# Performance work log

Hardware: AMD Instinct MI355X
Metric: run time of the kernel (lower is better)

The kernel has to match this reference:

```python
import jax, jax.numpy as jnp
import numpy as np

B, S, D = 4, 2048, 2048
H = 16
Q_LORA = 1536
KV_LORA = 512
D_NOPE = 128
D_ROPE = 64
D_V = 128
MLP = 8192
EPS = 1e-6
THETA = 10000.0


def rmsnorm(x, scale, eps=EPS):
    var = jnp.mean(jnp.square(x.astype(jnp.float32)), axis=-1, keepdims=True)
    return (x * jax.lax.rsqrt(var + eps)).astype(x.dtype) * scale


def rope(x, positions):
    # x: [B, S, H, d], positions: [B, S]
    d = x.shape[-1]
    inv_freq = 1.0 / (THETA ** (jnp.arange(0, d, 2, dtype=jnp.float32) / d))
    ang = positions.astype(jnp.float32)[..., None] * inv_freq  # [B,S,d/2]
    cos = jnp.cos(ang)[:, :, None, :]
    sin = jnp.sin(ang)[:, :, None, :]
    x1, x2 = jnp.split(x, 2, axis=-1)
    return jnp.concatenate([x1 * cos - x2 * sin, x2 * cos + x1 * sin], axis=-1)


def setup_inputs() -> dict:
    key = jax.random.key(0)
    ks = jax.random.split(key, 16)
    sd = lambda fan: 1.0 / np.sqrt(fan)
    inp = {
        'inputs': jax.random.normal(ks[0], (B, S, D), jnp.float32),
        'decoder_segment_ids': jnp.ones((B, S), jnp.int32),
        'decoder_positions': jnp.broadcast_to(jnp.arange(S, dtype=jnp.int32), (B, S)),
        'pre_ln_scale': jnp.ones((D,), jnp.float32),
        'post_ln_scale': jnp.ones((D,), jnp.float32),
        'q_ln_scale': jnp.ones((Q_LORA,), jnp.float32),
        'kv_ln_scale': jnp.ones((KV_LORA,), jnp.float32),
        'wq_a': jax.random.normal(ks[1], (D, Q_LORA), jnp.float32) * sd(D),
        'wq_b': jax.random.normal(ks[2], (Q_LORA, H, D_NOPE + D_ROPE), jnp.float32) * sd(Q_LORA),
        'wkv_a': jax.random.normal(ks[3], (D, KV_LORA + D_ROPE), jnp.float32) * sd(D),
        'wkv_b': jax.random.normal(ks[4], (KV_LORA, H, D_NOPE + D_V), jnp.float32) * sd(KV_LORA),
        'wo_attn': jax.random.normal(ks[5], (H, D_V, D), jnp.float32) * sd(H * D_V),
        'wi_0': jax.random.normal(ks[6], (D, MLP), jnp.float32) * sd(D),
        'wi_1': jax.random.normal(ks[7], (D, MLP), jnp.float32) * sd(D),
        'wo_mlp': jax.random.normal(ks[8], (MLP, D), jnp.float32) * sd(MLP),
    }
    return inp


def reference(inputs, decoder_segment_ids, decoder_positions, pre_ln_scale, post_ln_scale,
              q_ln_scale, kv_ln_scale, wq_a, wq_b, wkv_a, wkv_b, wo_attn, wi_0, wi_1, wo_mlp):
    # ---- pre-norm ----
    lnx = rmsnorm(inputs, pre_ln_scale)

    # ---- MLA attention ----
    # low-rank query: down-proj, norm, up-proj
    q_c = rmsnorm(lnx @ wq_a, q_ln_scale)                       # [B,S,Q_LORA]
    q = jnp.einsum('bsr,rhd->bshd', q_c, wq_b)                  # [B,S,H,nope+rope]
    q_nope, q_rope = q[..., :D_NOPE], q[..., D_NOPE:]

    # compressed kv + decoupled rope key
    kv = lnx @ wkv_a                                            # [B,S,KV_LORA+rope]
    c_kv = rmsnorm(kv[..., :KV_LORA], kv_ln_scale)
    k_rope = kv[..., KV_LORA:][:, :, None, :]                   # [B,S,1,rope]
    kvu = jnp.einsum('bsr,rhd->bshd', c_kv, wkv_b)              # [B,S,H,nope+v]
    k_nope, v = kvu[..., :D_NOPE], kvu[..., D_NOPE:]

    q_rope = rope(q_rope, decoder_positions)
    k_rope = rope(k_rope, decoder_positions)
    k_rope = jnp.broadcast_to(k_rope, (B, S, H, D_ROPE))

    qf = jnp.concatenate([q_nope, q_rope], axis=-1)             # [B,S,H,192]
    kf = jnp.concatenate([k_nope, k_rope], axis=-1)

    scale = 1.0 / np.sqrt(D_NOPE + D_ROPE)
    scores = jnp.einsum('bqhd,bkhd->bhqk', qf, kf) * scale      # [B,H,S,S]

    pos = decoder_positions
    seg = decoder_segment_ids
    mask = (pos[:, :, None] >= pos[:, None, :]) & (seg[:, :, None] == seg[:, None, :])
    scores = jnp.where(mask[:, None, :, :], scores, -1e9)
    probs = jax.nn.softmax(scores, axis=-1)

    attn = jnp.einsum('bhqk,bkhd->bqhd', probs, v)              # [B,S,H,D_V]
    attn_out = jnp.einsum('bqhd,hdm->bqm', attn, wo_attn)       # [B,S,D]

    # ---- residual + post-norm ----
    intermediate = inputs + attn_out
    hidden = rmsnorm(intermediate, post_ln_scale)

    # ---- gated MLP (silu * linear) ----
    mlp = (jax.nn.silu(hidden @ wi_0) * (hidden @ wi_1)) @ wo_mlp

    return mlp + intermediate
```

## Files before the change

kernel.cpp:

```cpp
#include <hip/hip_runtime.h>
#include <stdint.h>

typedef unsigned short u16;
typedef __bf16 bf16x8 __attribute__((ext_vector_type(8)));
typedef float f32x4 __attribute__((ext_vector_type(4)));

#define B_ 4
#define S_ 2048
#define H_ 16
#define TOK (B_*S_)
#define MFMA_B16 __builtin_amdgcn_mfma_f32_16x16x32_bf16

__device__ __forceinline__ u16 f32_bf16(float f) {
    union { float f; unsigned int u; } x; x.f = f;
    return (u16)((x.u + 0x7fffu + ((x.u >> 16) & 1u)) >> 16);
}
__device__ __forceinline__ float bf2f(u16 v) {
    union { unsigned int u; float f; } x; x.u = ((unsigned int)v) << 16; return x.f;
}
__device__ __forceinline__ void gld_lds16(const u16* g, u16* lds) {
    __builtin_amdgcn_global_load_lds(
        (const __attribute__((address_space(1))) unsigned int*)g,
        (__attribute__((address_space(3))) unsigned int*)lds, 16, 0, 0);
}

__global__ void fill_sentinel(float* o, int n) {
    int i = blockIdx.x * 256 + threadIdx.x;
    if (i < n) o[i] = 12345.0f;
}

__global__ __launch_bounds__(256) void transpose_f32_bf16(const float* __restrict__ in, u16* __restrict__ out,
                                                          int K, int N, int Npad) {
    __shared__ float t[32][33];
    int nb = blockIdx.x * 32, kb = blockIdx.y * 32;
    int c = threadIdx.x & 31, r = threadIdx.x >> 5;
#pragma unroll
    for (int i = 0; i < 4; ++i) {
        int kk = kb + r + i * 8, nn = nb + c;
        t[r + i * 8][c] = (kk < K && nn < N) ? in[(size_t)kk * N + nn] : 0.f;
    }
    __syncthreads();
#pragma unroll
    for (int i = 0; i < 4; ++i) {
        int no = nb + r + i * 8, ko = kb + c;
        if (no < Npad && ko < K) out[(size_t)no * K + ko] = f32_bf16(t[c][r + i * 8]);
    }
}

__global__ __launch_bounds__(256) void rmsnorm_f32(const float* __restrict__ in, const float* __restrict__ sc,
                                                   u16* __restrict__ out, int N) {
    int row = blockIdx.x;
    const float* x = in + (size_t)row * N;
    float ss = 0.f;
    for (int c = threadIdx.x * 4; c < N; c += 1024) {
        float4 v = *(const float4*)(x + c);
        ss += v.x * v.x + v.y * v.y + v.z * v.z + v.w * v.w;
    }
#pragma unroll
    for (int off = 32; off; off >>= 1) ss += __shfl_down(ss, off);
    __shared__ float red[4];
    if ((threadIdx.x & 63) == 0) red[threadIdx.x >> 6] = ss;
    __syncthreads();
    float rs = rsqrtf((red[0] + red[1] + red[2] + red[3]) / (float)N + 1e-6f);
    for (int c = threadIdx.x * 4; c < N; c += 1024) {
        float4 v = *(const float4*)(x + c);
        float4 s4 = *(const float4*)(sc + c);
        ushort4 ov;
        ov.x = f32_bf16(v.x * rs * s4.x);
        ov.y = f32_bf16(v.y * rs * s4.y);
        ov.z = f32_bf16(v.z * rs * s4.z);
        ov.w = f32_bf16(v.w * rs * s4.w);
        *(ushort4*)&out[(size_t)row * N + c] = ov;
    }
}

__global__ __launch_bounds__(256) void rmsnorm_bf16(const u16* __restrict__ in, const float* __restrict__ sc,
                                                    u16* __restrict__ out, int N) {
    int row = blockIdx.x;
    const u16* x = in + (size_t)row * N;
    float ss = 0.f;
    for (int c = threadIdx.x * 8; c < N; c += 2048) {
        ushort4 v0 = *(const ushort4*)(x + c);
        ushort4 v1 = *(const ushort4*)(x + c + 4);
        float f0 = bf2f(v0.x), f1 = bf2f(v0.y), f2 = bf2f(v0.z), f3 = bf2f(v0.w);
        float f4 = bf2f(v1.x), f5 = bf2f(v1.y), f6 = bf2f(v1.z), f7 = bf2f(v1.w);
        ss += f0*f0 + f1*f1 + f2*f2 + f3*f3 + f4*f4 + f5*f5 + f6*f6 + f7*f7;
    }
#pragma unroll
    for (int off = 32; off; off >>= 1) ss += __shfl_down(ss, off);
    __shared__ float red[4];
    if ((threadIdx.x & 63) == 0) red[threadIdx.x >> 6] = ss;
    __syncthreads();
    float rs = rsqrtf((red[0] + red[1] + red[2] + red[3]) / (float)N + 1e-6f);
    for (int c = threadIdx.x * 8; c < N; c += 2048) {
        ushort4 v0 = *(const ushort4*)(x + c);
        ushort4 v1 = *(const ushort4*)(x + c + 4);
        ushort4 o0, o1;
        o0.x = f32_bf16(bf2f(v0.x) * rs * sc[c + 0]);
        o0.y = f32_bf16(bf2f(v0.y) * rs * sc[c + 1]);
        o0.z = f32_bf16(bf2f(v0.z) * rs * sc[c + 2]);
        o0.w = f32_bf16(bf2f(v0.w) * rs * sc[c + 3]);
        o1.x = f32_bf16(bf2f(v1.x) * rs * sc[c + 4]);
        o1.y = f32_bf16(bf2f(v1.y) * rs * sc[c + 5]);
        o1.z = f32_bf16(bf2f(v1.z) * rs * sc[c + 6]);
        o1.w = f32_bf16(bf2f(v1.w) * rs * sc[c + 7]);
        *(ushort4*)&out[(size_t)row * N + c] = o0;
        *(ushort4*)&out[(size_t)row * N + c + 4] = o1;
    }
}

__global__ __launch_bounds__(128) void kv_post(const u16* __restrict__ kv, const float* __restrict__ scale,
                                               const int* __restrict__ pos, u16* __restrict__ ckv,
                                               u16* __restrict__ kr) {
    int row = blockIdx.x;
    const u16* x = kv + (size_t)row * 640;
    int c = threadIdx.x * 4;
    ushort4 v = *(const ushort4*)(x + c);
    float f0 = bf2f(v.x), f1 = bf2f(v.y), f2 = bf2f(v.z), f3 = bf2f(v.w);
    float ss = f0*f0 + f1*f1 + f2*f2 + f3*f3;
#pragma unroll
    for (int off = 32; off; off >>= 1) ss += __shfl_down(ss, off);
    __shared__ float red[2];
    if ((threadIdx.x & 63) == 0) red[threadIdx.x >> 6] = ss;
    __syncthreads();
    float rs = rsqrtf((red[0] + red[1]) * (1.f / 512.f) + 1e-6f);
    float4 s4 = *(const float4*)(scale + c);
    ushort4 ov;
    ov.x = f32_bf16(f0 * rs * s4.x);
    ov.y = f32_bf16(f1 * rs * s4.y);
    ov.z = f32_bf16(f2 * rs * s4.z);
    ov.w = f32_bf16(f3 * rs * s4.w);
    *(ushort4*)&ckv[(size_t)row * 512 + c] = ov;
    if (threadIdx.x < 32) {
        int i = threadIdx.x;
        float x1 = bf2f(x[512 + i]), x2 = bf2f(x[544 + i]);
        float inv = expf(-(float)(2 * i) * (1.f / 64.f) * 9.2103403719761836f);
        float ang = (float)pos[row] * inv;
        float sn, cs; sincosf(ang, &sn, &cs);
        kr[(size_t)row * 64 + i]      = f32_bf16(x1 * cs - x2 * sn);
        kr[(size_t)row * 64 + 32 + i] = f32_bf16(x2 * cs + x1 * sn);
    }
}

__global__ __launch_bounds__(64) void q_rope_inplace(u16* __restrict__ q, const int* __restrict__ pos) {
    int token = blockIdx.x, h = blockIdx.y;
    u16* p = q + ((size_t)token * 16 + h) * 192;
    int t = threadIdx.x, i = t & 31;
    float x1 = bf2f(p[128 + i]), x2 = bf2f(p[160 + i]);
    float inv = expf(-(float)(2 * i) * (1.f / 64.f) * 9.2103403719761836f);
    float ang = (float)pos[token] * inv;
    float sn, cs; sincosf(ang, &sn, &cs);
    float val = (t < 32) ? (x1 * cs - x2 * sn) : (x2 * cs + x1 * sn);
    p[128 + t] = f32_bf16(val);
}

__global__ __launch_bounds__(320) void kv_build(const u16* __restrict__ kvu, const u16* __restrict__ kr,
                                                u16* __restrict__ kf, u16* __restrict__ vf, int tok0) {
    int local = blockIdx.x, h = blockIdx.y;
    int token = tok0 + local;
    int b = token >> 11, s = token & 2047;
    int bh = b * 16 + h;
    int tile = s >> 6, ki = s & 63;
    const u16* u = kvu + ((size_t)local * 16 + h) * 256;
    int t = threadIdx.x;
    if (t < 192) {
        u16 val = (t < 128) ? u[t] : kr[(size_t)token * 64 + (t - 128)];
        int byte = (ki * 384 + t * 2) ^ ((ki & 7) << 4);
        kf[(size_t)bh * (S_ * 192) + (size_t)tile * 12288 + (byte >> 1)] = val;
    } else {
        int dv = t - 192;
        u16 val = u[128 + dv];
        int byte = (dv * 128 + ki * 2) ^ ((dv & 7) << 4);
        vf[(size_t)bh * (S_ * 128) + (size_t)tile * 8192 + (byte >> 1)] = val;
    }
}

__global__ __launch_bounds__(256) void gemm128(const u16* __restrict__ A, const u16* __restrict__ Bt,
                                               u16* __restrict__ C, int M, int N, int K) {
    __shared__ u16 As[128 * 32];
    __shared__ u16 Bs[128 * 32];
    const int l = threadIdx.x & 63, w = threadIdx.x >> 6;
    const int wr = w >> 1, wc = w & 1;
    const int m0 = blockIdx.y * 128, n0 = blockIdx.x * 128;
    const int lm = l & 15, lg = l >> 4;
    const int srow = l >> 2, sk = (l & 3) * 8;
    f32x4 acc[4][4] = {};
    for (int k0 = 0; k0 < K; k0 += 32) {
#pragma unroll
        for (int i = 0; i < 2; ++i) {
            int c = w * 2 + i;
            gld_lds16(A  + (size_t)(m0 + c * 16 + srow) * K + k0 + sk, &As[c * 512]);
            gld_lds16(Bt + (size_t)(n0 + c * 16 + srow) * K + k0 + sk, &Bs[c * 512]);
        }
        __syncthreads();
        bf16x8 a[4], b[4];
#pragma unroll
        for (int m = 0; m < 4; ++m) a[m] = *(const bf16x8*)&As[(wr * 64 + m * 16 + lm) * 32 + lg * 8];
#pragma unroll
        for (int n = 0; n < 4; ++n) b[n] = *(const bf16x8*)&Bs[(wc * 64 + n * 16 + lm) * 32 + lg * 8];
#pragma unroll
        for (int m = 0; m < 4; ++m)
#pragma unroll
            for (int n = 0; n < 4; ++n)
                acc[m][n] = MFMA_B16(a[m], b[n], acc[m][n], 0, 0, 0);
        __syncthreads();
    }
#pragma unroll
    for (int m = 0; m < 4; ++m)
#pragma unroll
        for (int j = 0; j < 4; ++j) {
            int row = m0 + wr * 64 + m * 16 + lg * 4 + j;
            size_t base = (size_t)row * N + n0 + wc * 64;
#pragma unroll
            for (int n = 0; n < 4; ++n)
                C[base + n * 16 + lm] = f32_bf16(acc[m][n][j]);
        }
}

template<int EPI>
__global__ __launch_bounds__(512, 2) void gemm256(const u16* __restrict__ A, const u16* __restrict__ Bt,
                                                  void* __restrict__ Cv, const void* __restrict__ Rv,
                                                  int M, int N, int K) {
    __shared__ u16 lds[65536];
    char* ldsb = (char*)lds;
    const int tid = threadIdx.x;
    const int l = tid & 63, w = tid >> 6;
    const int wr = w >> 2, wcn = w & 3;
    const int lm = l & 15, lg = l >> 4;
    const int m0 = blockIdx.y * 256, n0 = blockIdx.x * 256;

    int gm[2], gk[2];
#pragma unroll
    for (int ld = 0; ld < 2; ++ld) {
        int P = tid * 16 + ld * 8192;
        int row = P >> 7;
        int un = (P & 127) ^ ((row & 7) << 4);
        gm[ld] = row * 2 + (un >> 6);
        gk[ld] = (un & 63) >> 1;
    }
    const u16* Ab = A + (size_t)m0 * K;
    const u16* Bb = Bt + (size_t)n0 * K;

    f32x4 acc[8][4] = {};

    auto stageA = [&](int t) {
#pragma unroll
        for (int ld = 0; ld < 2; ++ld)
            gld_lds16(Ab + (size_t)gm[ld] * K + t * 32 + gk[ld],
                      (u16*)(ldsb + (t & 3) * 32768 + tid * 16 + ld * 8192));
    };
    auto stageB = [&](int t) {
#pragma unroll
        for (int ld = 0; ld < 2; ++ld)
            gld_lds16(Bb + (size_t)gm[ld] * K + t * 32 + gk[ld],
                      (u16*)(ldsb + (t & 3) * 32768 + 16384 + tid * 16 + ld * 8192));
    };
    auto readA = [&](int buf, int fm) -> bf16x8 {
        int m = wr * 128 + fm * 16 + lm;
        int off = ((m & 1) * 64 + lg * 16) ^ (((m >> 1) & 7) << 4);
        return *(const bf16x8*)(ldsb + buf * 32768 + (m >> 1) * 128 + off);
    };
    auto readB = [&](int buf, int fn) -> bf16x8 {
        int n = wcn * 64 + fn * 16 + lm;
        int off = ((n & 1) * 64 + lg * 16) ^ (((n >> 1) & 7) << 4);
        return *(const bf16x8*)(ldsb + buf * 32768 + 16384 + (n >> 1) * 128 + off);
    };

    const int ntile = K >> 5;
    stageA(0); stageB(0);
    stageA(1); stageB(1);
    stageA(2); stageB(2);
    asm volatile("s_waitcnt vmcnt(8)" ::: "memory");
    __builtin_amdgcn_s_barrier();

#pragma unroll 1
    for (int t = 0; t < ntile; ++t) {
        const int buf = t & 3;
        bf16x8 b0 = readB(buf, 0), b1 = readB(buf, 1), b2 = readB(buf, 2), b3 = readB(buf, 3);
        bf16x8 a0 = readA(buf, 0), a1 = readA(buf, 1), a2 = readA(buf, 2), a3 = readA(buf, 3);
        if (t + 3 < ntile) stageA(t + 3);
        asm volatile("s_waitcnt lgkmcnt(0)" ::: "memory");
        __builtin_amdgcn_s_barrier();
        __builtin_amdgcn_sched_barrier(0);
        __builtin_amdgcn_s_setprio(1);
        acc[0][0] = MFMA_B16(a0, b0, acc[0][0], 0, 0, 0);
        acc[0][1] = MFMA_B16(a0, b1, acc[0][1], 0, 0, 0);
        acc[0][2] = MFMA_B16(a0, b2, acc[0][2], 0, 0, 0);
        acc[0][3] = MFMA_B16(a0, b3, acc[0][3], 0, 0, 0);
        acc[1][0] = MFMA_B16(a1, b0, acc[1][0], 0, 0, 0);
        acc[1][1] = MFMA_B16(a1, b1, acc[1][1], 0, 0, 0);
        acc[1][2] = MFMA_B16(a1, b2, acc[1][2], 0, 0, 0);
        acc[1][3] = MFMA_B16(a1, b3, acc[1][3], 0, 0, 0);
        acc[2][0] = MFMA_B16(a2, b0, acc[2][0], 0, 0, 0);
        acc[2][1] = MFMA_B16(a2, b1, acc[2][1], 0, 0, 0);
        acc[2][2] = MFMA_B16(a2, b2, acc[2][2], 0, 0, 0);
        acc[2][3] = MFMA_B16(a2, b3, acc[2][3], 0, 0, 0);
        acc[3][0] = MFMA_B16(a3, b0, acc[3][0], 0, 0, 0);
        acc[3][1] = MFMA_B16(a3, b1, acc[3][1], 0, 0, 0);
        acc[3][2] = MFMA_B16(a3, b2, acc[3][2], 0, 0, 0);
        acc[3][3] = MFMA_B16(a3, b3, acc[3][3], 0, 0, 0);
        __builtin_amdgcn_s_setprio(0);
        __builtin_amdgcn_s_barrier();
        a0 = readA(buf, 4); a1 = readA(buf, 5); a2 = readA(buf, 6); a3 = readA(buf, 7);
        if (t + 3 < ntile) stageB(t + 3);
        asm volatile("s_waitcnt lgkmcnt(0)" ::: "memory");
        if (t < ntile - 3)       { asm volatile("s_waitcnt vmcnt(8)" ::: "memory"); }
        else if (t == ntile - 3) { asm volatile("s_waitcnt vmcnt(4)" ::: "memory"); }
        else if (t == ntile - 2) { asm volatile("s_waitcnt vmcnt(0)" ::: "memory"); }
        __builtin_amdgcn_s_barrier();
        __builtin_amdgcn_sched_barrier(0);
        __builtin_amdgcn_s_setprio(1);
        acc[4][0] = MFMA_B16(a0, b0, acc[4][0], 0, 0, 0);
        acc[4][1] = MFMA_B16(a0, b1, acc[4][1], 0, 0, 0);
        acc[4][2] = MFMA_B16(a0, b2, acc[4][2], 0, 0, 0);
        acc[4][3] = MFMA_B16(a0, b3, acc[4][3], 0, 0, 0);
        acc[5][0] = MFMA_B16(a1, b0, acc[5][0], 0, 0, 0);
        acc[5][1] = MFMA_B16(a1, b1, acc[5][1], 0, 0, 0);
        acc[5][2] = MFMA_B16(a1, b2, acc[5][2], 0, 0, 0);
        acc[5][3] = MFMA_B16(a1, b3, acc[5][3], 0, 0, 0);
        acc[6][0] = MFMA_B16(a2, b0, acc[6][0], 0, 0, 0);
        acc[6][1] = MFMA_B16(a2, b1, acc[6][1], 0, 0, 0);
        acc[6][2] = MFMA_B16(a2, b2, acc[6][2], 0, 0, 0);
        acc[6][3] = MFMA_B16(a2, b3, acc[6][3], 0, 0, 0);
        acc[7][0] = MFMA_B16(a3, b0, acc[7][0], 0, 0, 0);
        acc[7][1] = MFMA_B16(a3, b1, acc[7][1], 0, 0, 0);
        acc[7][2] = MFMA_B16(a3, b2, acc[7][2], 0, 0, 0);
        acc[7][3] = MFMA_B16(a3, b3, acc[7][3], 0, 0, 0);
        __builtin_amdgcn_s_setprio(0);
        __builtin_amdgcn_s_barrier();
    }
#pragma unroll
    for (int fm = 0; fm < 8; ++fm)
#pragma unroll
        for (int j = 0; j < 4; ++j) {
            int row = m0 + wr * 128 + fm * 16 + lg * 4 + j;
            size_t base = (size_t)row * N + n0 + wcn * 64;
#pragma unroll
            for (int fn = 0; fn < 4; ++fn) {
                size_t idx = base + fn * 16 + lm;
                float v = acc[fm][fn][j];
                if (EPI == 0) {
                    ((u16*)Cv)[idx] = f32_bf16(v);
                } else if (EPI == 1) {
                    ((float*)Cv)[idx] = v + ((const float*)Rv)[idx];
                } else {
                    float x0 = bf2f(((const u16*)Rv)[idx]);
                    float sl = x0 / (1.f + expf(-x0));
                    ((u16*)Cv)[idx] = f32_bf16(sl * v);
                }
            }
        }
}

__global__ __launch_bounds__(256) void attn_fwd(const u16* __restrict__ qf, const u16* __restrict__ kfs,
                                                const u16* __restrict__ vfs, u16* __restrict__ attn) {
    __shared__ u16 Ks[64 * 192];
    __shared__ u16 Vs[128 * 64];
    __shared__ u16 Ps[4][1024];
    const int px = blockIdx.x;
    const int bh = blockIdx.y;
    const int b = bh >> 4, h = bh & 15;
    const int l = threadIdx.x & 63, w = threadIdx.x >> 6;
    const int lm = l & 15, g = l >> 4;
    const u16* kb0 = kfs + (size_t)bh * (S_ * 192);
    const u16* vb0 = vfs + (size_t)bh * (S_ * 128);
    const float scale = 0.07216878364870322f;

    for (int pass = 0; pass < 2; ++pass) {
        const int qb = pass ? (31 - px) : px;
        const int qrow = qb * 64 + w * 16 + lm;
        const u16* qp = qf + (((size_t)(b * S_ + qrow)) * 16 + h) * 192 + g * 8;
        bf16x8 qr[6];
#pragma unroll
        for (int c = 0; c < 6; ++c) qr[c] = *(const bf16x8*)(qp + c * 32);
        f32x4 o[8] = {};
        float mrow[4] = {-1e30f, -1e30f, -1e30f, -1e30f};
        float lrow[4] = {0.f, 0.f, 0.f, 0.f};
        for (int kt = 0; kt <= qb; ++kt) {
            const u16* kc = kb0 + (size_t)kt * 12288;
            const u16* vc = vb0 + (size_t)kt * 8192;
#pragma unroll
            for (int i = 0; i < 6; ++i) {
                int c = w + i * 4;
                gld_lds16(kc + c * 512 + l * 8, &Ks[c * 512]);
            }
#pragma unroll
            for (int i = 0; i < 4; ++i) {
                int c = w + i * 4;
                gld_lds16(vc + c * 512 + l * 8, &Vs[c * 512]);
            }
            __syncthreads();
            f32x4 sc[4] = {};
#pragma unroll
            for (int nf = 0; nf < 4; ++nf) {
                int key = nf * 16 + lm;
                int kswz = (key & 7) << 4;
#pragma unroll
                for (int c = 0; c < 6; ++c) {
                    int byte = (key * 384 + (c * 32 + g * 8) * 2) ^ kswz;
                    bf16x8 kv = *(const bf16x8*)((const char*)Ks + byte);
                    sc[nf] = MFMA_B16(qr[c], kv, sc[nf], 0, 0, 0);
                }
            }
#pragma unroll
            for (int j = 0; j < 4; ++j) {
                const int q_g = qb * 64 + w * 16 + g * 4 + j;
                float mx = -1e30f;
#pragma unroll
                for (int nf = 0; nf < 4; ++nf) {
                    int key_g = kt * 64 + nf * 16 + lm;
                    float v = sc[nf][j] * scale;
                    v = (key_g > q_g) ? -1e30f : v;
                    sc[nf][j] = v;
                    mx = fmaxf(mx, v);
                }
                mx = fmaxf(mx, __shfl_xor(mx, 1));
                mx = fmaxf(mx, __shfl_xor(mx, 2));
                mx = fmaxf(mx, __shfl_xor(mx, 4));
                mx = fmaxf(mx, __shfl_xor(mx, 8));
                float newm = fmaxf(mrow[j], mx);
                float fac = __expf(mrow[j] - newm);
                mrow[j] = newm;
                float rs = 0.f;
                u16 pb[4];
#pragma unroll
                for (int nf = 0; nf < 4; ++nf) {
                    float pv = __expf(sc[nf][j] - newm);
                    rs += pv;
                    pb[nf] = f32_bf16(pv);
                }
                rs += __shfl_xor(rs, 1);
                rs += __shfl_xor(rs, 2);
                rs += __shfl_xor(rs, 4);
                rs += __shfl_xor(rs, 8);
                lrow[j] = lrow[j] * fac + rs;
#pragma unroll
                for (int n = 0; n < 8; ++n) o[n][j] *= fac;
                int row = g * 4 + j;
                int rswz = (row & 7) << 4;
#pragma unroll
                for (int nf = 0; nf < 4; ++nf) {
                    int byte = (row * 128 + (nf * 16 + lm) * 2) ^ rswz;
                    *(u16*)((char*)&Ps[w][0] + byte) = pb[nf];
                }
            }
#pragma unroll
            for (int kc2 = 0; kc2 < 2; ++kc2) {
                int pbyte = (lm * 128 + (kc2 * 32 + g * 8) * 2) ^ ((lm & 7) << 4);
                bf16x8 pa = *(const bf16x8*)((const char*)&Ps[w][0] + pbyte);
#pragma unroll
                for (int n = 0; n < 8; ++n) {
                    int dv = n * 16 + lm;
                    int vbyte = (dv * 128 + (kc2 * 32 + g * 8) * 2) ^ ((dv & 7) << 4);
                    bf16x8 vv = *(const bf16x8*)((const char*)Vs + vbyte);
                    o[n] = MFMA_B16(pa, vv, o[n], 0, 0, 0);
                }
            }
            __syncthreads();
        }
#pragma unroll
        for (int j = 0; j < 4; ++j) {
            float inv = 1.f / lrow[j];
            int s = qb * 64 + w * 16 + g * 4 + j;
            size_t base = ((size_t)(b * S_ + s)) * (H_ * 128) + h * 128;
#pragma unroll
            for (int n = 0; n < 8; ++n)
                attn[base + n * 16 + lm] = f32_bf16(o[n][j] * inv);
        }
    }
}

extern "C" void kernel_launch(void* const* d_in, const int* in_sizes, int n_in,
                              void* d_out, int out_size, void* d_ws, size_t ws_size,
                              hipStream_t stream) {
    (void)in_sizes; (void)n_in;
    const float* inputs = (const float*)d_in[0];
    const int*   pos    = (const int*)d_in[2];
    const float* pre_s  = (const float*)d_in[3];
    const float* post_s = (const float*)d_in[4];
    const float* q_s    = (const float*)d_in[5];
    const float* kv_s   = (const float*)d_in[6];
    const float* wq_a   = (const float*)d_in[7];
    const float* wq_b   = (const float*)d_in[8];
    const float* wkv_a  = (const float*)d_in[9];
    const float* wkv_b  = (const float*)d_in[10];
    const float* wo_at  = (const float*)d_in[11];
    const float* wi0    = (const float*)d_in[12];
    const float* wi1    = (const float*)d_in[13];
    const float* wom    = (const float*)d_in[14];
    float* out = (float*)d_out;

    char* p = (char*)d_ws;
    auto alloc = [&](size_t n) { char* r = p; p += (n + 255) & ~(size_t)255; return r; };
    char* R1   = alloc((size_t)134217728);
    u16* vf    = (u16*)alloc((size_t)33554432);
    u16* aslot = (u16*)alloc((size_t)33554432);
    u16* wslot = (u16*)alloc((size_t)33554432);
    u16* ckv   = (u16*)alloc((size_t)8388608);
    u16* krope = (u16*)alloc((size_t)1048576);
    if ((size_t)(p - (char*)d_ws) > ws_size) {
        fill_sentinel<<<(out_size + 255) / 256, 256, 0, stream>>>(out, out_size);
        return;
    }
    u16* kf    = (u16*)R1;
    u16* q_c   = (u16*)R1;
    u16* kvtmp = (u16*)(R1 + 25165824);
    u16* q     = (u16*)(R1 + 50331648);
    u16* lnx   = (u16*)(R1 + 100663296);
    u16* kvu   = (u16*)(R1 + 100663296);
    u16* X     = (u16*)R1;

    rmsnorm_f32<<<TOK, 256, 0, stream>>>(inputs, pre_s, lnx, 2048);
    transpose_f32_bf16<<<dim3(48, 64), 256, 0, stream>>>(wq_a, wslot, 2048, 1536, 1536);
    gemm256<0><<<dim3(6, 32), 512, 0, stream>>>(lnx, wslot, q_c, nullptr, TOK, 1536, 2048);
    rmsnorm_bf16<<<TOK, 256, 0, stream>>>(q_c, q_s, q_c, 1536);
    transpose_f32_bf16<<<dim3(20, 64), 256, 0, stream>>>(wkv_a, wslot, 2048, 576, 640);
    gemm128<<<dim3(5, 64), 256, 0, stream>>>(lnx, wslot, kvtmp, TOK, 640, 2048);
    kv_post<<<TOK, 128, 0, stream>>>(kvtmp, kv_s, pos, ckv, krope);
    transpose_f32_bf16<<<dim3(96, 48), 256, 0, stream>>>(wq_b, wslot, 1536, 3072, 3072);
    gemm256<0><<<dim3(12, 32), 512, 0, stream>>>(q_c, wslot, q, nullptr, TOK, 3072, 1536);
    q_rope_inplace<<<dim3(TOK, 16), 64, 0, stream>>>(q, pos);
    transpose_f32_bf16<<<dim3(128, 16), 256, 0, stream>>>(wkv_b, wslot, 512, 4096, 4096);
    for (int ch = 0; ch < 2; ++ch) {
        int t0 = ch * 4096;
        gemm256<0><<<dim3(16, 16), 512, 0, stream>>>(ckv + (size_t)t0 * 512, wslot, kvu, nullptr, 4096, 4096, 512);
        kv_build<<<dim3(4096, 16), 320, 0, stream>>>(kvu, krope, kf, vf, t0);
    }
    attn_fwd<<<dim3(16, 64), 256, 0, stream>>>(q, kf, vf, aslot);
    transpose_f32_bf16<<<dim3(64, 64), 256, 0, stream>>>(wo_at, wslot, 2048, 2048, 2048);
    gemm256<1><<<dim3(8, 32), 512, 0, stream>>>(aslot, wslot, out, inputs, TOK, 2048, 2048);
    rmsnorm_f32<<<TOK, 256, 0, stream>>>(out, post_s, aslot, 2048);
    transpose_f32_bf16<<<dim3(256, 64), 256, 0, stream>>>(wi0, wslot, 2048, 8192, 8192);
    gemm256<0><<<dim3(32, 32), 512, 0, stream>>>(aslot, wslot, X, nullptr, TOK, 8192, 2048);
    transpose_f32_bf16<<<dim3(256, 64), 256, 0, stream>>>(wi1, wslot, 2048, 8192, 8192);
    gemm256<2><<<dim3(32, 32), 512, 0, stream>>>(aslot, wslot, X, X, TOK, 8192, 2048);
    transpose_f32_bf16<<<dim3(64, 256), 256, 0, stream>>>(wom, wslot, 8192, 2048, 2048);
    gemm256<1><<<dim3(8, 32), 512, 0, stream>>>(X, wslot, out, out, TOK, 2048, 8192);
}
```

Baseline: 1.736 ms.

## Double-buffer K/V tiles in attention and collapse GEMM loop to one barrier

The attention kernel now keeps two LDS buffers for K and V and prefetches the next key tile while computing the current one, which hides global-to-LDS latency that was previously fully exposed before each tile. The GEMM main loop is restructured to a single wait and barrier per K-tile, issuing both A and B prefetches up front and reading all eight A fragments before running the 32 MFMAs, dropping the setprio hints and the mid-tile barrier. Exchanges: more LDS per attention block (may lower occupancy) and higher register pressure in the GEMM from holding eight A fragments. The vmcnt accounting also changes, so the synchronisation correctness depends on the counts matching the outstanding loads.

Result: slower. 1.801 ms (+3.7%).

```diff
diff --git a/kernel.cpp b/kernel.cpp
--- a/kernel.cpp
+++ b/kernel.cpp
@@ -270,19 +270,19 @@
     stageA(0); stageB(0);
     stageA(1); stageB(1);
     stageA(2); stageB(2);
-    asm volatile("s_waitcnt vmcnt(8)" ::: "memory");
-    __builtin_amdgcn_s_barrier();
 
 #pragma unroll 1
     for (int t = 0; t < ntile; ++t) {
         const int buf = t & 3;
+        if (t + 2 < ntile)      { asm volatile("s_waitcnt vmcnt(8)" ::: "memory"); }
+        else if (t + 1 < ntile) { asm volatile("s_waitcnt vmcnt(4)" ::: "memory"); }
+        else                    { asm volatile("s_waitcnt vmcnt(0)" ::: "memory"); }
+        __builtin_amdgcn_s_barrier();
+        __builtin_amdgcn_sched_barrier(0);
+        if (t + 3 < ntile) { stageA(t + 3); stageB(t + 3); }
         bf16x8 b0 = readB(buf, 0), b1 = readB(buf, 1), b2 = readB(buf, 2), b3 = readB(buf, 3);
         bf16x8 a0 = readA(buf, 0), a1 = readA(buf, 1), a2 = readA(buf, 2), a3 = readA(buf, 3);
-        if (t + 3 < ntile) stageA(t + 3);
-        asm volatile("s_waitcnt lgkmcnt(0)" ::: "memory");
-        __builtin_amdgcn_s_barrier();
-        __builtin_amdgcn_sched_barrier(0);
-        __builtin_amdgcn_s_setprio(1);
+        bf16x8 a4 = readA(buf, 4), a5 = readA(buf, 5), a6 = readA(buf, 6), a7 = readA(buf, 7);
         acc[0][0] = MFMA_B16(a0, b0, acc[0][0], 0, 0, 0);
         acc[0][1] = MFMA_B16(a0, b1, acc[0][1], 0, 0, 0);
         acc[0][2] = MFMA_B16(a0, b2, acc[0][2], 0, 0, 0);
@@ -299,35 +299,22 @@
         acc[3][1] = MFMA_B16(a3, b1, acc[3][1], 0, 0, 0);
         acc[3][2] = MFMA_B16(a3, b2, acc[3][2], 0, 0, 0);
         acc[3][3] = MFMA_B16(a3, b3, acc[3][3], 0, 0, 0);
-        __builtin_amdgcn_s_setprio(0);
-        __builtin_amdgcn_s_barrier();
-        a0 = readA(buf, 4); a1 = readA(buf, 5); a2 = readA(buf, 6); a3 = readA(buf, 7);
-        if (t + 3 < ntile) stageB(t + 3);
-        asm volatile("s_waitcnt lgkmcnt(0)" ::: "memory");
-        if (t < ntile - 3)       { asm volatile("s_waitcnt vmcnt(8)" ::: "memory"); }
-        else if (t == ntile - 3) { asm volatile("s_waitcnt vmcnt(4)" ::: "memory"); }
-        else if (t == ntile - 2) { asm volatile("s_waitcnt vmcnt(0)" ::: "memory"); }
-        __builtin_amdgcn_s_barrier();
-        __builtin_amdgcn_sched_barrier(0);
-        __builtin_amdgcn_s_setprio(1);
-        acc[4][0] = MFMA_B16(a0, b0, acc[4][0], 0, 0, 0);
-        acc[4][1] = MFMA_B16(a0, b1, acc[4][1], 0, 0, 0);
-        acc[4][2] = MFMA_B16(a0, b2, acc[4][2], 0, 0, 0);
-        acc[4][3] = MFMA_B16(a0, b3, acc[4][3], 0, 0, 0);
-        acc[5][0] = MFMA_B16(a1, b0, acc[5][0], 0, 0, 0);
-        acc[5][1] = MFMA_B16(a1, b1, acc[5][1], 0, 0, 0);
-        acc[5][2] = MFMA_B16(a1, b2, acc[5][2], 0, 0, 0);
-        acc[5][3] = MFMA_B16(a1, b3, acc[5][3], 0, 0, 0);
-        acc[6][0] = MFMA_B16(a2, b0, acc[6][0], 0, 0, 0);
-        acc[6][1] = MFMA_B16(a2, b1, acc[6][1], 0, 0, 0);
-        acc[6][2] = MFMA_B16(a2, b2, acc[6][2], 0, 0, 0);
-        acc[6][3] = MFMA_B16(a2, b3, acc[6][3], 0, 0, 0);
-        acc[7][0] = MFMA_B16(a3, b0, acc[7][0], 0, 0, 0);
-        acc[7][1] = MFMA_B16(a3, b1, acc[7][1], 0, 0, 0);
-        acc[7][2] = MFMA_B16(a3, b2, acc[7][2], 0, 0, 0);
-        acc[7][3] = MFMA_B16(a3, b3, acc[7][3], 0, 0, 0);
-        __builtin_amdgcn_s_setprio(0);
-        __builtin_amdgcn_s_barrier();
+        acc[4][0] = MFMA_B16(a4, b0, acc[4][0], 0, 0, 0);
+        acc[4][1] = MFMA_B16(a4, b1, acc[4][1], 0, 0, 0);
+        acc[4][2] = MFMA_B16(a4, b2, acc[4][2], 0, 0, 0);
+        acc[4][3] = MFMA_B16(a4, b3, acc[4][3], 0, 0, 0);
+        acc[5][0] = MFMA_B16(a5, b0, acc[5][0], 0, 0, 0);
+        acc[5][1] = MFMA_B16(a5, b1, acc[5][1], 0, 0, 0);
+        acc[5][2] = MFMA_B16(a5, b2, acc[5][2], 0, 0, 0);
+        acc[5][3] = MFMA_B16(a5, b3, acc[5][3], 0, 0, 0);
+        acc[6][0] = MFMA_B16(a6, b0, acc[6][0], 0, 0, 0);
+        acc[6][1] = MFMA_B16(a6, b1, acc[6][1], 0, 0, 0);
+        acc[6][2] = MFMA_B16(a6, b2, acc[6][2], 0, 0, 0);
+        acc[6][3] = MFMA_B16(a6, b3, acc[6][3], 0, 0, 0);
+        acc[7][0] = MFMA_B16(a7, b0, acc[7][0], 0, 0, 0);
+        acc[7][1] = MFMA_B16(a7, b1, acc[7][1], 0, 0, 0);
+        acc[7][2] = MFMA_B16(a7, b2, acc[7][2], 0, 0, 0);
+        acc[7][3] = MFMA_B16(a7, b3, acc[7][3], 0, 0, 0);
     }
 #pragma unroll
     for (int fm = 0; fm < 8; ++fm)
@@ -354,8 +341,8 @@
 
 __global__ __launch_bounds__(256) void attn_fwd(const u16* __restrict__ qf, const u16* __restrict__ kfs,
                                                 const u16* __restrict__ vfs, u16* __restrict__ attn) {
-    __shared__ u16 Ks[64 * 192];
-    __shared__ u16 Vs[128 * 64];
+    __shared__ u16 Ks[2][64 * 192];
+    __shared__ u16 Vs[2][128 * 64];
     __shared__ u16 Ps[4][1024];
     const int px = blockIdx.x;
     const int bh = blockIdx.y;
@@ -366,6 +353,21 @@
     const u16* vb0 = vfs + (size_t)bh * (S_ * 128);
     const float scale = 0.07216878364870322f;
 
+    auto stageKV = [&](int kt2, int d2) {
+        const u16* kc = kb0 + (size_t)kt2 * 12288;
+        const u16* vc = vb0 + (size_t)kt2 * 8192;
+#pragma unroll
+        for (int i = 0; i < 6; ++i) {
+            int c = w + i * 4;
+            gld_lds16(kc + c * 512 + l * 8, &Ks[d2][c * 512]);
+        }
+#pragma unroll
+        for (int i = 0; i < 4; ++i) {
+            int c = w + i * 4;
+            gld_lds16(vc + c * 512 + l * 8, &Vs[d2][c * 512]);
+        }
+    };
+
     for (int pass = 0; pass < 2; ++pass) {
         const int qb = pass ? (31 - px) : px;
         const int qrow = qb * 64 + w * 16 + lm;
@@ -376,20 +378,12 @@
         f32x4 o[8] = {};
         float mrow[4] = {-1e30f, -1e30f, -1e30f, -1e30f};
         float lrow[4] = {0.f, 0.f, 0.f, 0.f};
+        __syncthreads();
+        stageKV(0, 0);
         for (int kt = 0; kt <= qb; ++kt) {
-            const u16* kc = kb0 + (size_t)kt * 12288;
-            const u16* vc = vb0 + (size_t)kt * 8192;
-#pragma unroll
-            for (int i = 0; i < 6; ++i) {
-                int c = w + i * 4;
-                gld_lds16(kc + c * 512 + l * 8, &Ks[c * 512]);
-            }
-#pragma unroll
-            for (int i = 0; i < 4; ++i) {
-                int c = w + i * 4;
-                gld_lds16(vc + c * 512 + l * 8, &Vs[c * 512]);
-            }
+            const int d = kt & 1;
             __syncthreads();
+            if (kt < qb) stageKV(kt + 1, d ^ 1);
             f32x4 sc[4] = {};
 #pragma unroll
             for (int nf = 0; nf < 4; ++nf) {
@@ -398,7 +392,7 @@
 #pragma unroll
                 for (int c = 0; c < 6; ++c) {
                     int byte = (key * 384 + (c * 32 + g * 8) * 2) ^ kswz;
-                    bf16x8 kv = *(const bf16x8*)((const char*)Ks + byte);
+                    bf16x8 kv = *(const bf16x8*)((const char*)&Ks[d][0] + byte);
                     sc[nf] = MFMA_B16(qr[c], kv, sc[nf], 0, 0, 0);
                 }
             }
@@ -452,11 +446,10 @@
                 for (int n = 0; n < 8; ++n) {
                     int dv = n * 16 + lm;
                     int vbyte = (dv * 128 + (kc2 * 32 + g * 8) * 2) ^ ((dv & 7) << 4);
-                    bf16x8 vv = *(const bf16x8*)((const char*)Vs + vbyte);
+                    bf16x8 vv = *(const bf16x8*)((const char*)&Vs[d][0] + vbyte);
                     o[n] = MFMA_B16(pa, vv, o[n], 0, 0, 0);
                 }
             }
-            __syncthreads();
         }
 #pragma unroll
         for (int j = 0; j < 4; ++j) {
```
